# Kernel optimization log

Hardware: AMD Instinct MI355X
Metric: run time of the kernel (lower is better)

## Reference

```python
import jax, jax.numpy as jnp
import numpy as np

EPS = 1e-5
ND, NDIS, NP, NG, NPW = 40000, 40000, 80000, 80000, 40000
D = 128


def gcn(x_src, src, dst, n_dst, W, b):
    # DGL GraphConv with norm='both': D_dst^{-1/2} A^T D_src^{-1/2} X W + b
    deg_out = jnp.maximum(jnp.zeros((x_src.shape[0],), x_src.dtype).at[src].add(1.0), 1.0)
    xs = x_src * (deg_out ** -0.5)[:, None]
    msg = jax.ops.segment_sum(xs[src], dst, num_segments=n_dst)
    deg_in = jnp.maximum(jnp.zeros((n_dst,), x_src.dtype).at[dst].add(1.0), 1.0)
    return (msg * (deg_in ** -0.5)[:, None]) @ W + b


def bn_prelu(v, gamma, beta, a):
    # BatchNorm1d (training-mode batch stats, biased var) then PReLU (scalar slope)
    mu = v.mean(0)
    var = v.var(0)
    y = gamma * (v - mu) / jnp.sqrt(var + EPS) + beta
    return jnp.where(y >= 0, y, a * y)


def sem_att(z, W1, b1, w2):
    # z: [N, K, D]; shared SemanticAttention across node types
    s = jnp.tanh(z @ W1 + b1) @ w2        # [N, K]
    beta = jax.nn.softmax(s.mean(0))       # [K]
    return jnp.einsum('k,nkd->nd', beta, z)


def setup_inputs():
    key = jax.random.key(0)
    ks = iter(jax.random.split(key, 40))
    f = lambda n: jax.random.normal(next(ks), (n, D), jnp.float32)
    inp = {'h_drug': f(ND), 'h_disease': f(NDIS), 'h_protein': f(NP),
           'h_gene': f(NG), 'h_pathway': f(NPW)}
    rels = {'dd': (ND, ND, 640000), 'ddi': (ND, NDIS, 640000), 'disdis': (NDIS, NDIS, 640000),
            'dp': (ND, NP, 640000), 'pp': (NP, NP, 1280000), 'pg': (NP, NG, 1280000),
            'gg': (NG, NG, 1280000), 'gpw': (NG, NPW, 1280000), 'pwpw': (NPW, NPW, 640000),
            'pwdis': (NPW, NDIS, 640000)}
    for name, (ns, nd, E) in rels.items():
        inp[name + '_src'] = jax.random.randint(next(ks), (E,), 0, ns)
        inp[name + '_dst'] = jax.random.randint(next(ks), (E,), 0, nd)
    inp['W_blocks'] = jax.random.normal(next(ks), (5, 3, D, D), jnp.float32) * 0.09
    inp['b_blocks'] = jnp.zeros((5, 3, D), jnp.float32)
    inp['bn_gamma'] = jnp.ones((5, D), jnp.float32)
    inp['bn_beta'] = jnp.zeros((5, D), jnp.float32)
    inp['prelu_a'] = jnp.full((5,), 0.25, jnp.float32)
    inp['attn_W1'] = jax.random.normal(next(ks), (D, D), jnp.float32) * 0.09
    inp['attn_b1'] = jnp.zeros((D,), jnp.float32)
    inp['attn_w2'] = jax.random.normal(next(ks), (D,), jnp.float32) * 0.09
    return inp


def reference(h_drug, h_disease, h_protein, h_gene, h_pathway,
              dd_src, dd_dst, ddi_src, ddi_dst, disdis_src, disdis_dst,
              dp_src, dp_dst, pp_src, pp_dst, pg_src, pg_dst,
              gg_src, gg_dst, gpw_src, gpw_dst, pwpw_src, pwpw_dst,
              pwdis_src, pwdis_dst,
              W_blocks, b_blocks, bn_gamma, bn_beta, prelu_a,
              attn_W1, attn_b1, attn_w2):
    act = lambda i, v: bn_prelu(v, bn_gamma[i], bn_beta[i], prelu_a[i])
    # block 0: drug_disease  (rels: drug_drug, drug_disease, disease_disease)
    d0 = act(0, gcn(h_drug, dd_src, dd_dst, ND, W_blocks[0, 0], b_blocks[0, 0]))
    dis0 = act(0, gcn(h_drug, ddi_src, ddi_dst, NDIS, W_blocks[0, 1], b_blocks[0, 1])
               + gcn(h_disease, disdis_src, disdis_dst, NDIS, W_blocks[0, 2], b_blocks[0, 2]))
    # block 1: drug_protein
    d1 = act(1, gcn(h_drug, dd_src, dd_dst, ND, W_blocks[1, 0], b_blocks[1, 0]))
    p1 = act(1, gcn(h_drug, dp_src, dp_dst, NP, W_blocks[1, 1], b_blocks[1, 1])
             + gcn(h_protein, pp_src, pp_dst, NP, W_blocks[1, 2], b_blocks[1, 2]))
    # block 2: protein_gene
    p2 = act(2, gcn(h_protein, pp_src, pp_dst, NP, W_blocks[2, 0], b_blocks[2, 0]))
    g2 = act(2, gcn(h_protein, pg_src, pg_dst, NG, W_blocks[2, 1], b_blocks[2, 1])
             + gcn(h_gene, gg_src, gg_dst, NG, W_blocks[2, 2], b_blocks[2, 2]))
    # block 3: gene_pathway
    g3 = act(3, gcn(h_gene, gg_src, gg_dst, NG, W_blocks[3, 0], b_blocks[3, 0]))
    pw3 = act(3, gcn(h_gene, gpw_src, gpw_dst, NPW, W_blocks[3, 1], b_blocks[3, 1])
              + gcn(h_pathway, pwpw_src, pwpw_dst, NPW, W_blocks[3, 2], b_blocks[3, 2]))
    # block 4: pathway_disease
    pw4 = act(4, gcn(h_pathway, pwpw_src, pwpw_dst, NPW, W_blocks[4, 0], b_blocks[4, 0]))
    dis4 = act(4, gcn(h_pathway, pwdis_src, pwdis_dst, NDIS, W_blocks[4, 1], b_blocks[4, 1])
               + gcn(h_disease, disdis_src, disdis_dst, NDIS, W_blocks[4, 2], b_blocks[4, 2]))
    att = lambda a, b: sem_att(jnp.stack([a, b], axis=1), attn_W1, attn_b1, attn_w2)
    return (att(d0, d1), att(dis0, dis4), att(p1, p2), att(g2, g3), att(pw3, pw4))
```

## Files before the change

kernel.cpp:

```cpp
#include <hip/hip_runtime.h>
#include <hip/hip_bf16.h>

#define D128 128

typedef __attribute__((ext_vector_type(8))) short bf16x8;
typedef __attribute__((ext_vector_type(4))) float f32x4;

__device__ inline unsigned short f2bf(float f) {
    unsigned u = __float_as_uint(f);
    u = u + 0x7fffu + ((u >> 16) & 1u);
    return (unsigned short)(u >> 16);
}
__device__ inline float bf2f(unsigned short h) {
    return __uint_as_float(((unsigned)h) << 16);
}
__device__ inline float fast_tanh(float x) {
    float e = __expf(2.f * x);
    return 1.f - 2.f * __builtin_amdgcn_rcpf(e + 1.f);
}

__device__ __forceinline__ void stage_w(const unsigned short* __restrict__ Wt,
                                        unsigned short* lw, int t)
{
    const uint4* srcW = (const uint4*)Wt;
    uint4* dstW = (uint4*)lw;
    for (int i = t; i < 2048; i += 256) {
        int row = i >> 4, sl = i & 15;
        dstW[row * 16 + (sl ^ (row & 7))] = srcW[i];
    }
}
__device__ __forceinline__ bf16x8 read_w(const unsigned short* lw, int row, int kt, int lq)
{
    int slot = (kt * 4 + lq) ^ (row & 7);
    return *(const bf16x8*)(lw + row * 128 + slot * 8);
}

__device__ __forceinline__ void wave_scan(const int* arr, int* ofs, int n, int lane)
{
    int k = (n + 63) >> 6;
    int base = lane * k;
    int sum = 0;
    for (int i = 0; i < k; i++) { int idx = base + i; if (idx < n) sum += arr[idx]; }
    int pre = sum;
    for (int off = 1; off < 64; off <<= 1) {
        int u = __shfl(pre, (lane - off) & 63);
        if (lane >= off) pre += u;
    }
    int run = pre - sum;
    for (int i = 0; i < k; i++) { int idx = base + i; if (idx < n) { ofs[idx] = run; run += arr[idx]; } }
    if (lane == 63) ofs[n] = run;
}

__global__ __launch_bounds__(256) void xconv_scaled(
    const float* __restrict__ in, const int* __restrict__ degs,
    unsigned* __restrict__ out, int nrows)
{
    int t = threadIdx.x;
    int lane = t & 63, rr = t >> 6;
    int row = blockIdx.x * 4 + rr;
    if (row >= nrows) return;
    float sc = rsqrtf((float)max(degs[row], 1));
    float2 v = ((const float2*)(in + (size_t)row * 128))[lane];
    out[(size_t)row * 64 + lane] =
        (unsigned)f2bf(v.x * sc) | ((unsigned)f2bf(v.y * sc) << 16);
}

__global__ void wconv_t(const float* __restrict__ W_blocks, const float* __restrict__ W1,
                        unsigned short* __restrict__ wt)
{
    int m = blockIdx.x;
    const float* src = (m < 15) ? (W_blocks + (size_t)m * 16384) : W1;
    unsigned short* dst = wt + (size_t)m * 16384;
    for (int i = threadIdx.x; i < 16384; i += 256) {
        int n = i >> 7, k = i & 127;
        dst[i] = f2bf(src[k * 128 + n]);
    }
}

struct BuildArgs {
    const int* esrc[10]; const int* edst[10];
    int* histD; int* histS;
    int cumBlk[11]; int dstColBase[11]; int srcColBase[11]; int E[10];
};

__global__ __launch_bounds__(256) void part_count(BuildArgs A)
{
    __shared__ int hd[160], hs[320];
    int blk = blockIdx.x, t = threadIdx.x;
    int r = 0;
    while (r < 9 && blk >= A.cumBlk[r + 1]) r++;
    int blkInRel = blk - A.cumBlk[r];
    int nbD = A.dstColBase[r + 1] - A.dstColBase[r];
    int nbS = A.srcColBase[r + 1] - A.srcColBase[r];
    for (int i = t; i < nbD; i += 256) hd[i] = 0;
    for (int i = t; i < nbS; i += 256) hs[i] = 0;
    __syncthreads();
    int e0 = blkInRel * 16384;
    const int* sp = A.esrc[r];
    const int* dp = A.edst[r];
    int E = A.E[r];
#pragma unroll 4
    for (int j = 0; j < 64; j++) {
        int e = e0 + j * 256 + t;
        if (e < E) {
            atomicAdd(&hd[dp[e] >> 9], 1);
            atomicAdd(&hs[sp[e] >> 8], 1);
        }
    }
    __syncthreads();
    int cd = A.dstColBase[r], cs = A.srcColBase[r];
    for (int i = t; i < nbD; i += 256)
        A.histD[(size_t)(cd + i) * 80 + blkInRel] = hd[i];
    for (int i = t; i < nbS; i += 256)
        A.histS[(size_t)(cs + i) * 80 + blkInRel] = hs[i];
}

struct ScanArgs { int* hist; int* totals; int colBase[11]; int cumBlk[11]; };

__global__ __launch_bounds__(256) void col_scan(ScanArgs A)
{
    __shared__ int v[80];
    int col = blockIdx.x, t = threadIdx.x;
    int r = 0;
    while (r < 9 && col >= A.colBase[r + 1]) r++;
    int nblk = A.cumBlk[r + 1] - A.cumBlk[r];
    for (int i = t; i < nblk; i += 256) v[i] = A.hist[(size_t)col * 80 + i];
    __syncthreads();
    if (t == 0) {
        int run = 0;
        for (int i = 0; i < nblk; i++) { int c = v[i]; v[i] = run; run += c; }
        A.totals[col] = run;
    }
    __syncthreads();
    for (int i = t; i < nblk; i += 256) A.hist[(size_t)col * 80 + i] = v[i];
}

__global__ __launch_bounds__(256) void base_scan(const int* __restrict__ totals,
                                                 int* __restrict__ colbase, int n)
{
    __shared__ int v[2200];
    int t = threadIdx.x;
    for (int i = t; i < n; i += 256) v[i] = totals[i];
    __syncthreads();
    if (t == 0) {
        int run = 0;
        for (int i = 0; i < n; i++) { int c = v[i]; v[i] = run; run += c; }
        v[n] = run;
    }
    __syncthreads();
    for (int i = t; i <= n; i += 256) colbase[i] = v[i];
}

struct ScatArgs {
    const int* esrc[10]; const int* edst[10];
    const int* histD; const int* colbaseD;
    const int* histS; const int* colbaseS;
    int* epart; unsigned char* spart;
    int cumBlk[11]; int dstColBase[11]; int srcColBase[11]; int E[10];
};

__global__ __launch_bounds__(256) void scatter_all(ScatArgs A)
{
    __shared__ int stageE[4096];
    __shared__ unsigned short bidS[4096];
    __shared__ unsigned char bidE[4096];
    __shared__ unsigned char stageS[4096];
    __shared__ int gbaseD[160], gcurD[160], lhistD[160], lofsD[161];
    __shared__ int gbaseS[320], gcurS[320], lhistS[320], lofsS[321];

    int blk = blockIdx.x, t = threadIdx.x;
    int r = 0;
    while (r < 9 && blk >= A.cumBlk[r + 1]) r++;
    int blkInRel = blk - A.cumBlk[r];
    int cd = A.dstColBase[r], cs = A.srcColBase[r];
    int nbD = A.dstColBase[r + 1] - cd;
    int nbS = A.srcColBase[r + 1] - cs;
    for (int i = t; i < nbD; i += 256) {
        gbaseD[i] = A.colbaseD[cd + i] + A.histD[(size_t)(cd + i) * 80 + blkInRel];
        gcurD[i] = 0;
    }
    for (int i = t; i < nbS; i += 256) {
        gbaseS[i] = A.colbaseS[cs + i] + A.histS[(size_t)(cs + i) * 80 + blkInRel];
        gcurS[i] = 0;
    }
    const int* sp = A.esrc[r];
    const int* dp = A.edst[r];
    int E = A.E[r];
    int blkbase = blkInRel * 16384;

    for (int c = 0; c < 4; c++) {
        int e0 = blkbase + c * 4096;
        int sv[16], dv[16];
#pragma unroll
        for (int j = 0; j < 16; j++) {
            int e = e0 + j * 256 + t;
            sv[j] = (e < E) ? sp[e] : -1;
            dv[j] = (e < E) ? dp[e] : 0;
        }
        for (int i = t; i < nbD; i += 256) lhistD[i] = 0;
        for (int i = t; i < nbS; i += 256) lhistS[i] = 0;
        __syncthreads();
#pragma unroll
        for (int j = 0; j < 16; j++) {
            if (sv[j] >= 0) {
                atomicAdd(&lhistD[dv[j] >> 9], 1);
                atomicAdd(&lhistS[sv[j] >> 8], 1);
            }
        }
        __syncthreads();
        if (t < 64) wave_scan(lhistD, lofsD, nbD, t);
        else if (t < 128) wave_scan(lhistS, lofsS, nbS, t - 64);
        __syncthreads();
        for (int i = t; i < nbD; i += 256) lhistD[i] = 0;
        for (int i = t; i < nbS; i += 256) lhistS[i] = 0;
        __syncthreads();
#pragma unroll
        for (int j = 0; j < 16; j++) {
            if (sv[j] >= 0) {
                int bd = dv[j] >> 9;
                int p = atomicAdd(&lhistD[bd], 1);
                int ix = lofsD[bd] + p;
                stageE[ix] = (sv[j] & 0x1FFFF) | ((dv[j] & 511) << 17);
                bidE[ix] = (unsigned char)bd;
                int bs = sv[j] >> 8;
                int q = atomicAdd(&lhistS[bs], 1);
                int iy = lofsS[bs] + q;
                stageS[iy] = (unsigned char)(sv[j] & 255);
                bidS[iy] = (unsigned short)bs;
            }
        }
        __syncthreads();
        int cntv = lofsD[nbD];
        for (int i = t; i < cntv; i += 256) {
            int b = bidE[i];
            A.epart[gbaseD[b] + gcurD[b] + i - lofsD[b]] = stageE[i];
        }
        for (int i = t; i < cntv; i += 256) {
            int b = bidS[i];
            A.spart[(size_t)gbaseS[b] + gcurS[b] + i - lofsS[b]] = stageS[i];
        }
        __syncthreads();
        for (int i = t; i < nbD; i += 256) gcurD[i] += lofsD[i + 1] - lofsD[i];
        for (int i = t; i < nbS; i += 256) gcurS[i] += lofsS[i + 1] - lofsS[i];
        __syncthreads();
    }
}

struct FillArgs {
    const int* epart; const int* colbase;
    int* cursor; int* ebuf; int* oflow;
    int colBase[11];
    int cursorBase[10]; int ebufBase[10]; int cap[10]; int nd[10];
};

__global__ __launch_bounds__(256) void bucket_fill(FillArgs A)
{
    __shared__ int lcur[512];
    int col = blockIdx.x, t = threadIdx.x;
    int r = 0;
    while (r < 9 && col >= A.colBase[r + 1]) r++;
    int b = col - A.colBase[r];
    for (int i = t; i < 512; i += 256) lcur[i] = 0;
    __syncthreads();
    int start = A.colbase[col], end = A.colbase[col + 1];
    int cap = A.cap[r];
    int* eb = A.ebuf + (size_t)A.ebufBase[r];
    int* ofl = A.oflow + r * 8194;
    for (int i = start + t; i < end; i += 256) {
        int v = A.epart[i];
        int s = v & 0x1FFFF;
        int dlow = (v >> 17) & 511;
        int p = atomicAdd(&lcur[dlow], 1);
        if (p < cap) eb[(size_t)(b * 512 + dlow) * cap + p] = s;
        else {
            int q = atomicAdd(&ofl[0], 1);
            if (q < 4095) { ofl[2 + 2 * q] = b * 512 + dlow; ofl[3 + 2 * q] = s; }
        }
    }
    __syncthreads();
    for (int i = t; i < 512; i += 256) {
        int d = b * 512 + i;
        if (d < A.nd[r]) A.cursor[A.cursorBase[r] + d] = lcur[i];
    }
}

struct DegArgs {
    const unsigned char* spart; const int* colbase;
    int* degs;
    int colBase[11]; int degsBase[10]; int ns[10];
};

__global__ __launch_bounds__(256) void deg_count(DegArgs A)
{
    __shared__ int lc[256];
    int col = blockIdx.x, t = threadIdx.x;
    int r = 0;
    while (r < 9 && col >= A.colBase[r + 1]) r++;
    int b = col - A.colBase[r];
    lc[t] = 0;
    __syncthreads();
    int start = A.colbase[col], end = A.colbase[col + 1];
    for (int i = start + t; i < end; i += 256)
        atomicAdd(&lc[A.spart[i]], 1);
    __syncthreads();
    int s = b * 256 + t;
    if (s < A.ns[r]) A.degs[A.degsBase[r] + s] = lc[t];
}

__global__ __launch_bounds__(256) void gather_bf16(
    const unsigned* __restrict__ Xb,
    const int* __restrict__ cursor, const int* __restrict__ ebuf,
    const int* __restrict__ oflow, unsigned* __restrict__ aggb, int nd, int cap)
{
    int t = threadIdx.x;
    int lane = t & 63, r = t >> 6;
    int d = blockIdx.x * 4 + r;
    if (d >= nd) return;
    int cnt = cursor[d];
    int end = min(cnt, cap);
    const int* eb = ebuf + (size_t)d * cap;
    float a0 = 0.f, a1 = 0.f;
    int i = 0;
    for (; i + 4 <= end; i += 4) {
        int s0 = eb[i], s1 = eb[i + 1], s2 = eb[i + 2], s3 = eb[i + 3];
        unsigned x0 = Xb[(size_t)s0 * 64 + lane];
        unsigned x1 = Xb[(size_t)s1 * 64 + lane];
        unsigned x2 = Xb[(size_t)s2 * 64 + lane];
        unsigned x3 = Xb[(size_t)s3 * 64 + lane];
        a0 += bf2f((unsigned short)(x0 & 0xffff)) + bf2f((unsigned short)(x1 & 0xffff))
            + bf2f((unsigned short)(x2 & 0xffff)) + bf2f((unsigned short)(x3 & 0xffff));
        a1 += bf2f((unsigned short)(x0 >> 16)) + bf2f((unsigned short)(x1 >> 16))
            + bf2f((unsigned short)(x2 >> 16)) + bf2f((unsigned short)(x3 >> 16));
    }
    for (; i < end; i++) {
        int s0 = eb[i];
        unsigned x0 = Xb[(size_t)s0 * 64 + lane];
        a0 += bf2f((unsigned short)(x0 & 0xffff));
        a1 += bf2f((unsigned short)(x0 >> 16));
    }
    if (cnt > cap) {
        int n = min(oflow[0], 4095);
        for (int ii = 0; ii < n; ii++) {
            if (oflow[2 + 2 * ii] == d) {
                int s0 = oflow[3 + 2 * ii];
                unsigned x0 = Xb[(size_t)s0 * 64 + lane];
                a0 += bf2f((unsigned short)(x0 & 0xffff));
                a1 += bf2f((unsigned short)(x0 >> 16));
            }
        }
    }
    float sc = rsqrtf((float)max(cnt, 1));
    a0 *= sc; a1 *= sc;
    aggb[(size_t)d * 64 + lane] = (unsigned)f2bf(a0) | ((unsigned)f2bf(a1) << 16);
}

__device__ __forceinline__ void epi_store(
    f32x4* acc, unsigned short* __restrict__ Vb, int accum, int do_stats,
    float* ssum, float* ssq, int row0, int lr, int lq)
{
#pragma unroll
    for (int n = 0; n < 8; n++) {
        int col = n * 16 + lr;
        float s_ = 0.f, q_ = 0.f;
#pragma unroll
        for (int reg = 0; reg < 4; reg++) {
            int row = row0 + lq * 4 + reg;
            float v = acc[n][reg];
            unsigned short* vp = &Vb[(size_t)row * D128 + col];
            if (accum) v += bf2f(*vp);
            *vp = f2bf(v);
            s_ += v; q_ += v * v;
        }
        if (do_stats) {
            s_ += __shfl_xor(s_, 16); s_ += __shfl_xor(s_, 32);
            q_ += __shfl_xor(q_, 16); q_ += __shfl_xor(q_, 32);
            if (lq == 0) {
                atomicAdd(&ssum[col], s_);
                atomicAdd(&ssq[col], q_);
            }
        }
    }
}

__global__ __launch_bounds__(256) void gemm_mfma(
    const unsigned short* __restrict__ A, const unsigned short* __restrict__ Wt,
    unsigned short* __restrict__ Vb, int accum, int do_stats, float* __restrict__ statsraw)
{
    __shared__ unsigned short lw[16384];
    __shared__ float ssum[128], ssq[128];
    int t = threadIdx.x;
    int wave = t >> 6, lane = t & 63;
    int lr = lane & 15, lq = lane >> 4;
    int row0 = blockIdx.x * 64 + wave * 16;

    if (t < 128) { ssum[t] = 0.f; ssq[t] = 0.f; }
    stage_w(Wt, lw, t);
    __syncthreads();

    f32x4 acc[8];
#pragma unroll
    for (int n = 0; n < 8; n++) acc[n] = (f32x4)(0.f);

    const unsigned short* arow = A + (size_t)(row0 + lr) * 128 + lq * 8;
#pragma unroll
    for (int kt = 0; kt < 4; kt++) {
        bf16x8 af = *(const bf16x8*)(arow + kt * 32);
#pragma unroll
        for (int n = 0; n < 8; n++) {
            bf16x8 bfr = read_w(lw, n * 16 + lr, kt, lq);
            acc[n] = __builtin_amdgcn_mfma_f32_16x16x32_bf16(af, bfr, acc[n], 0, 0, 0);
        }
    }
    epi_store(acc, Vb, accum, do_stats, ssum, ssq, row0, lr, lq);
    if (do_stats) {
        __syncthreads();
        if (t < 128) atomicAdd(&statsraw[t], ssum[t]);
        else atomicAdd(&statsraw[t], ssq[t - 128]);
    }
}

__global__ __launch_bounds__(256) void gemm_mfma2(
    const unsigned short* __restrict__ A,
    const unsigned short* __restrict__ Wt0, const unsigned short* __restrict__ Wt1,
    unsigned short* __restrict__ V0b, unsigned short* __restrict__ V1b,
    int acc0f, int acc1f, int st0, int st1,
    float* __restrict__ sr0, float* __restrict__ sr1)
{
    __shared__ unsigned short lw0[16384], lw1[16384];
    __shared__ float ssum0[128], ssq0[128], ssum1[128], ssq1[128];
    int t = threadIdx.x;
    int wave = t >> 6, lane = t & 63;
    int lr = lane & 15, lq = lane >> 4;
    int row0 = blockIdx.x * 64 + wave * 16;

    if (t < 128) { ssum0[t] = 0.f; ssq0[t] = 0.f; ssum1[t] = 0.f; ssq1[t] = 0.f; }
    stage_w(Wt0, lw0, t);
    stage_w(Wt1, lw1, t);
    __syncthreads();

    f32x4 acc0[8], acc1[8];
#pragma unroll
    for (int n = 0; n < 8; n++) { acc0[n] = (f32x4)(0.f); acc1[n] = (f32x4)(0.f); }

    const unsigned short* arow = A + (size_t)(row0 + lr) * 128 + lq * 8;
#pragma unroll
    for (int kt = 0; kt < 4; kt++) {
        bf16x8 af = *(const bf16x8*)(arow + kt * 32);
#pragma unroll
        for (int n = 0; n < 8; n++) {
            int row = n * 16 + lr;
            bf16x8 b0 = read_w(lw0, row, kt, lq);
            bf16x8 b1 = read_w(lw1, row, kt, lq);
            acc0[n] = __builtin_amdgcn_mfma_f32_16x16x32_bf16(af, b0, acc0[n], 0, 0, 0);
            acc1[n] = __builtin_amdgcn_mfma_f32_16x16x32_bf16(af, b1, acc1[n], 0, 0, 0);
        }
    }
    epi_store(acc0, V0b, acc0f, st0, ssum0, ssq0, row0, lr, lq);
    epi_store(acc1, V1b, acc1f, st1, ssum1, ssq1, row0, lr, lq);
    __syncthreads();
    if (st0) {
        if (t < 128) atomicAdd(&sr0[t], ssum0[t]);
        else atomicAdd(&sr0[t], ssq0[t - 128]);
    }
    if (st1) {
        if (t < 128) atomicAdd(&sr1[t], ssum1[t]);
        else atomicAdd(&sr1[t], ssq1[t - 128]);
    }
}

struct FinArgs { int Ms[10]; };

__global__ void bn_finalize(const float* __restrict__ raw, float* __restrict__ fin, FinArgs fa)
{
    int tt = blockIdx.x;
    int c = threadIdx.x;
    float m = (float)fa.Ms[tt];
    float s = raw[tt * 256 + c], sq = raw[tt * 256 + 128 + c];
    float mu = s / m;
    float var = fmaxf(sq / m - mu * mu, 0.f);
    fin[tt * 256 + c] = mu;
    fin[tt * 256 + 128 + c] = rsqrtf(var + 1e-5f);
}

__global__ __launch_bounds__(256) void attn_t(
    const unsigned short* __restrict__ Vb, const float* __restrict__ raw, float Minv,
    const float* __restrict__ gam, const float* __restrict__ bet,
    const float* __restrict__ pa,
    const unsigned short* __restrict__ W1t, const float* __restrict__ b1,
    const float* __restrict__ w2, float* __restrict__ Sout)
{
    __shared__ float st[256];
    __shared__ float red[4];
    int t = threadIdx.x;
    if (t < 128) {
        float mu = raw[t] * Minv;
        float var = fmaxf(raw[128 + t] * Minv - mu * mu, 0.f);
        st[t] = mu;
        st[128 + t] = rsqrtf(var + 1e-5f);
    }
    __syncthreads();

    int wave = t >> 6, lane = t & 63;
    int lr = lane & 15, lq = lane >> 4;
    int row0 = blockIdx.x * 64 + wave * 16;
    float a = *pa;

    f32x4 acc[8];
#pragma unroll
    for (int n = 0; n < 8; n++) acc[n] = (f32x4)(0.f);

    const unsigned short* vrow = Vb + (size_t)(row0 + lr) * D128;
#pragma unroll
    for (int kt = 0; kt < 4; kt++) {
        int k0 = kt * 32 + lq * 8;
        bf16x8 vv = *(const bf16x8*)(vrow + k0);
        bf16x8 af;
#pragma unroll
        for (int jj = 0; jj < 8; jj++) {
            int cc = k0 + jj;
            float y = bf2f((unsigned short)vv[jj]);
            float yy = gam[cc] * (y - st[cc]) * st[128 + cc] + bet[cc];
            yy = yy >= 0.f ? yy : a * yy;
            af[jj] = (short)f2bf(yy);
        }
#pragma unroll
        for (int n = 0; n < 8; n++) {
            bf16x8 bfr = *(const bf16x8*)(W1t + (size_t)(n * 16 + lr) * 128 + k0);
            acc[n] = __builtin_amdgcn_mfma_f32_16x16x32_bf16(af, bfr, acc[n], 0, 0, 0);
        }
    }

    float thr = 0.f;
#pragma unroll
    for (int n = 0; n < 8; n++) {
        int col = n * 16 + lr;
        float bc = b1[col], wc = w2[col];
#pragma unroll
        for (int reg = 0; reg < 4; reg++)
            thr += fast_tanh(acc[n][reg] + bc) * wc;
    }
#pragma unroll
    for (int off = 1; off < 64; off <<= 1)
        thr += __shfl_xor(thr, off);
    if (lane == 0) red[wave] = thr;
    __syncthreads();
    if (t == 0) atomicAdd(Sout, red[0] + red[1] + red[2] + red[3]);
}

struct CombArgs {
    float* outp[5]; const unsigned short* va[5]; const unsigned short* vb[5];
    const float* stats; const float* gam; const float* bet; const float* pa; const float* S;
    int ta[5]; int tb[5]; int blka[5]; int blkb[5]; float invM[5]; int cum[6];
};

__global__ void combine_all(CombArgs D)
{
    int b = blockIdx.x, t = threadIdx.x;
    int p = 0;
    while (p < 4 && b >= D.cum[p + 1]) p++;
    size_t idx = (size_t)(b - D.cum[p]) * 256 + t;
    int c = (int)(idx & 127);
    float s0 = D.S[2 * p] * D.invM[p], s1 = D.S[2 * p + 1] * D.invM[p];
    float mx = fmaxf(s0, s1);
    float e0 = expf(s0 - mx), e1 = expf(s1 - mx);
    float inv = 1.f / (e0 + e1);
    float b0 = e0 * inv, b1w = e1 * inv;
    const float* sta = D.stats + D.ta[p] * 256;
    const float* stb = D.stats + D.tb[p] * 256;
    const float* ga = D.gam + D.blka[p] * 128;
    const float* ba = D.bet + D.blka[p] * 128;
    const float* gb = D.gam + D.blkb[p] * 128;
    const float* bb = D.bet + D.blkb[p] * 128;
    float aa = D.pa[D.blka[p]], ab = D.pa[D.blkb[p]];
    float va = bf2f(D.va[p][idx]);
    float vb = bf2f(D.vb[p][idx]);
    float ya = ga[c] * (va - sta[c]) * sta[128 + c] + ba[c];
    ya = ya >= 0.f ? ya : aa * ya;
    float yb = gb[c] * (vb - stb[c]) * stb[128 + c] + bb[c];
    yb = yb >= 0.f ? yb : ab * yb;
    D.outp[p][idx] = b0 * ya + b1w * yb;
}

extern "C" void kernel_launch(void* const* d_in, const int* in_sizes, int n_in,
                              void* d_out, int out_size, void* d_ws, size_t ws_size,
                              hipStream_t stream)
{
    const float* feats[5] = {
        (const float*)d_in[0], (const float*)d_in[1], (const float*)d_in[2],
        (const float*)d_in[3], (const float*)d_in[4]
    };
    const float* W_blocks = (const float*)d_in[25];
    const float* bn_gamma = (const float*)d_in[27];
    const float* bn_beta  = (const float*)d_in[28];
    const float* prelu_a  = (const float*)d_in[29];
    const float* attn_W1  = (const float*)d_in[30];
    const float* attn_b1  = (const float*)d_in[31];
    const float* attn_w2  = (const float*)d_in[32];
    float* out = (float*)d_out;

    unsigned* xbf  = (unsigned*)out;
    unsigned* aggb = (unsigned*)(out + 5120000);
    int*      ebuf = (int*)(out + 10240000);

    float* wsf = (float*)d_ws;
    unsigned short* wsvb = (unsigned short*)wsf;
    unsigned short* wtbf = (unsigned short*)(wsf + 35840000);
    int* degs     = (int*)(wsf + 35971072);
    int* cursor   = degs + 560000;
    int* oflow    = cursor + 560000;
    int* histD    = oflow + 81940;
    int* histS    = histD + 88160;
    int* colbaseD = histS + 175520;
    int* totalsD  = colbaseD + 1103;
    int* colbaseS = totalsD + 1102;
    int* totalsS  = colbaseS + 2195;
    int* epart    = totalsS + 2194;
    unsigned char* spart = (unsigned char*)(epart + 8960000);
    float* statsraw = (float*)(epart + 8960000 + 2240000);
    float* statsfin = statsraw + 2560;
    float* Ssum     = statsfin + 2560;
    size_t needed = ((size_t)((float*)(Ssum + 16) - wsf)) * 4;
    if (ws_size < needed) return;

    const int Mt[10]  = {40000, 40000, 40000, 40000, 80000, 80000, 80000, 80000, 40000, 40000};
    const int blk[10] = {0, 1, 0, 4, 1, 2, 2, 3, 3, 4};
    size_t offV[10];
    {
        size_t o = 0;
        for (int t = 0; t < 10; t++) { offV[t] = o; o += (size_t)Mt[t] * 128; }
    }
    unsigned short* Vb[10];
    for (int t = 0; t < 10; t++) Vb[t] = wsvb + offV[t];
    const size_t offT[5] = {0, 5120000, 10240000, 20480000, 30720000};

    const int relFeat[10] = {0, 0, 0, 1, 2, 2, 3, 3, 4, 4};
    const int relSrc[10]  = {5, 7, 11, 9, 13, 15, 17, 19, 21, 23};
    const int relNs[10]   = {40000, 40000, 40000, 40000, 80000, 80000, 80000, 80000, 40000, 40000};
    const int relNd[10]   = {40000, 40000, 80000, 40000, 80000, 80000, 80000, 40000, 40000, 40000};
    const int relE[10]    = {640000, 640000, 640000, 640000, 1280000,
                             1280000, 1280000, 1280000, 640000, 640000};
    const int relCap[10]  = {40, 40, 24, 40, 40, 40, 40, 56, 40, 40};
    const int cumBlk[11]  = {0, 40, 80, 120, 160, 239, 318, 397, 476, 516, 556};
    const int dstColBase[11] = {0, 79, 158, 315, 394, 551, 708, 865, 944, 1023, 1102};
    const int srcColBase[11] = {0, 157, 314, 471, 628, 941, 1254, 1567, 1880, 2037, 2194};
    const int degsBase[10]   = {0, 40000, 80000, 120000, 160000, 240000, 320000, 400000, 480000, 520000};
    const int cursorBase[10] = {0, 40000, 80000, 160000, 200000, 280000, 360000, 440000, 480000, 520000};
    const int ebufBase[10]   = {0, 1600000, 3200000, 5120000, 6720000, 9920000,
                                13120000, 16320000, 18560000, 20160000};

    struct GJob { int tid; int widx; int accum; int stats; };
    const int relNjob[10] = {2, 1, 1, 2, 2, 1, 2, 1, 2, 1};
    const GJob relJob[10][2] = {
        {{0,  0, 0, 1}, {1,  3, 0, 1}},
        {{2,  1, 0, 0}, {0,  0, 0, 0}},
        {{4,  4, 0, 0}, {0,  0, 0, 0}},
        {{2,  2, 1, 1}, {3, 14, 0, 0}},
        {{4,  5, 1, 1}, {5,  6, 0, 1}},
        {{6,  7, 0, 0}, {0,  0, 0, 0}},
        {{6,  8, 1, 1}, {7,  9, 0, 1}},
        {{8, 10, 0, 0}, {0,  0, 0, 0}},
        {{8, 11, 1, 1}, {9, 12, 0, 1}},
        {{3, 13, 1, 1}, {0,  0, 0, 0}},
    };
    const int doneCnt[10] = {2, 0, 0, 1, 2, 0, 2, 0, 2, 1};
    const int doneT[10][2] = {{0,1},{0,0},{0,0},{2,0},{4,5},{0,0},{6,7},{0,0},{8,9},{3,0}};

    wconv_t<<<16, 256, 0, stream>>>(W_blocks, attn_W1, wtbf);
    hipMemsetAsync(statsraw, 0, (2560 + 2560 + 16) * sizeof(float), stream);
    hipMemsetAsync(oflow, 0, (size_t)81940 * sizeof(int), stream);

    BuildArgs BA;
    ScanArgs  SAD, SAS;
    ScatArgs  CA;
    FillArgs  FA;
    DegArgs   DA;
    for (int r = 0; r < 10; r++) {
        BA.esrc[r] = (const int*)d_in[relSrc[r]];
        BA.edst[r] = (const int*)d_in[relSrc[r] + 1];
        BA.E[r] = relE[r];
        CA.esrc[r] = BA.esrc[r]; CA.edst[r] = BA.edst[r]; CA.E[r] = relE[r];
        FA.cursorBase[r] = cursorBase[r];
        FA.ebufBase[r] = ebufBase[r];
        FA.cap[r] = relCap[r];
        FA.nd[r] = relNd[r];
        DA.degsBase[r] = degsBase[r];
        DA.ns[r] = relNs[r];
    }
    for (int i = 0; i < 11; i++) {
        BA.cumBlk[i] = cumBlk[i]; BA.dstColBase[i] = dstColBase[i]; BA.srcColBase[i] = srcColBase[i];
        SAD.colBase[i] = dstColBase[i]; SAD.cumBlk[i] = cumBlk[i];
        SAS.colBase[i] = srcColBase[i]; SAS.cumBlk[i] = cumBlk[i];
        CA.cumBlk[i] = cumBlk[i]; CA.dstColBase[i] = dstColBase[i]; CA.srcColBase[i] = srcColBase[i];
        FA.colBase[i] = dstColBase[i];
        DA.colBase[i] = srcColBase[i];
    }
    BA.histD = histD; BA.histS = histS;
    SAD.hist = histD; SAD.totals = totalsD;
    SAS.hist = histS; SAS.totals = totalsS;
    CA.histD = histD; CA.colbaseD = colbaseD;
    CA.histS = histS; CA.colbaseS = colbaseS;
    CA.epart = epart; CA.spart = spart;
    FA.epart = epart; FA.colbase = colbaseD;
    FA.cursor = cursor; FA.ebuf = ebuf; FA.oflow = oflow;
    DA.spart = spart; DA.colbase = colbaseS; DA.degs = degs;

    part_count<<<556, 256, 0, stream>>>(BA);
    col_scan<<<1102, 256, 0, stream>>>(SAD);
    col_scan<<<2194, 256, 0, stream>>>(SAS);
    base_scan<<<1, 256, 0, stream>>>(totalsD, colbaseD, 1102);
    base_scan<<<1, 256, 0, stream>>>(totalsS, colbaseS, 2194);
    scatter_all<<<556, 256, 0, stream>>>(CA);
    bucket_fill<<<1102, 256, 0, stream>>>(FA);
    deg_count<<<2194, 256, 0, stream>>>(DA);

    for (int r = 0; r < 10; r++) {
        xconv_scaled<<<(relNs[r] + 3) / 4, 256, 0, stream>>>(
            feats[relFeat[r]], degs + degsBase[r], xbf, relNs[r]);
        gather_bf16<<<relNd[r] / 4, 256, 0, stream>>>(
            xbf, cursor + cursorBase[r],
            ebuf + (size_t)ebufBase[r], oflow + r * 8194, aggb, relNd[r], relCap[r]);
        if (relNjob[r] == 2) {
            const GJob& G0 = relJob[r][0];
            const GJob& G1 = relJob[r][1];
            gemm_mfma2<<<relNd[r] / 64, 256, 0, stream>>>(
                (const unsigned short*)aggb,
                wtbf + (size_t)G0.widx * 16384, wtbf + (size_t)G1.widx * 16384,
                Vb[G0.tid], Vb[G1.tid], G0.accum, G1.accum, G0.stats, G1.stats,
                statsraw + (size_t)G0.tid * 256, statsraw + (size_t)G1.tid * 256);
        } else {
            const GJob& G = relJob[r][0];
            gemm_mfma<<<relNd[r] / 64, 256, 0, stream>>>(
                (const unsigned short*)aggb, wtbf + (size_t)G.widx * 16384,
                Vb[G.tid], G.accum, G.stats, statsraw + (size_t)G.tid * 256);
        }
        for (int k = 0; k < doneCnt[r]; k++) {
            int t = doneT[r][k];
            attn_t<<<Mt[t] / 64, 256, 0, stream>>>(
                Vb[t], statsraw + (size_t)t * 256, 1.0f / Mt[t],
                bn_gamma + blk[t] * 128, bn_beta + blk[t] * 128, prelu_a + blk[t],
                wtbf + (size_t)15 * 16384, attn_b1, attn_w2, Ssum + t);
        }
    }

    FinArgs fa;
    for (int t = 0; t < 10; t++) fa.Ms[t] = Mt[t];
    bn_finalize<<<10, 128, 0, stream>>>(statsraw, statsfin, fa);

    CombArgs CD;
    CD.stats = statsfin; CD.gam = bn_gamma; CD.bet = bn_beta; CD.pa = prelu_a; CD.S = Ssum;
    CD.cum[0] = 0;
    for (int p = 0; p < 5; p++) {
        CD.outp[p] = out + offT[p];
        CD.va[p] = Vb[p * 2];
        CD.vb[p] = Vb[p * 2 + 1];
        CD.ta[p] = p * 2; CD.tb[p] = p * 2 + 1;
        CD.blka[p] = blk[p * 2]; CD.blkb[p] = blk[p * 2 + 1];
        CD.invM[p] = 1.0f / Mt[p * 2];
        CD.cum[p + 1] = CD.cum[p] + Mt[p * 2] / 2;
    }
    combine_all<<<CD.cum[5], 256, 0, stream>>>(CD);
}
```

Measured before the change: 1.548 ms.

## Fuse bucket fill into gather via per-block LDS counting sort of edges

```diff
diff --git a/kernel.cpp b/kernel.cpp
--- a/kernel.cpp
+++ b/kernel.cpp
@@ -2,6 +2,7 @@
 #include <hip/hip_bf16.h>
 
 #define D128 128
+#define STAGE 12288
 
 typedef __attribute__((ext_vector_type(8))) short bf16x8;
 typedef __attribute__((ext_vector_type(4))) float f32x4;
@@ -85,7 +86,7 @@
 
 __global__ __launch_bounds__(256) void part_count(BuildArgs A)
 {
-    __shared__ int hd[160], hs[320];
+    __shared__ int hd[320], hs[320];
     int blk = blockIdx.x, t = threadIdx.x;
     int r = 0;
     while (r < 9 && blk >= A.cumBlk[r + 1]) r++;
@@ -103,7 +104,7 @@
     for (int j = 0; j < 64; j++) {
         int e = e0 + j * 256 + t;
         if (e < E) {
-            atomicAdd(&hd[dp[e] >> 9], 1);
+            atomicAdd(&hd[dp[e] >> 8], 1);
             atomicAdd(&hs[sp[e] >> 8], 1);
         }
     }
@@ -162,10 +163,10 @@
 __global__ __launch_bounds__(256) void scatter_all(ScatArgs A)
 {
     __shared__ int stageE[4096];
+    __shared__ unsigned short bidE[4096];
     __shared__ unsigned short bidS[4096];
-    __shared__ unsigned char bidE[4096];
     __shared__ unsigned char stageS[4096];
-    __shared__ int gbaseD[160], gcurD[160], lhistD[160], lofsD[161];
+    __shared__ int gbaseD[320], gcurD[320], lhistD[320], lofsD[321];
     __shared__ int gbaseS[320], gcurS[320], lhistS[320], lofsS[321];
 
     int blk = blockIdx.x, t = threadIdx.x;
@@ -203,7 +204,7 @@
 #pragma unroll
         for (int j = 0; j < 16; j++) {
             if (sv[j] >= 0) {
-                atomicAdd(&lhistD[dv[j] >> 9], 1);
+                atomicAdd(&lhistD[dv[j] >> 8], 1);
                 atomicAdd(&lhistS[sv[j] >> 8], 1);
             }
         }
@@ -217,11 +218,11 @@
 #pragma unroll
         for (int j = 0; j < 16; j++) {
             if (sv[j] >= 0) {
-                int bd = dv[j] >> 9;
+                int bd = dv[j] >> 8;
                 int p = atomicAdd(&lhistD[bd], 1);
                 int ix = lofsD[bd] + p;
-                stageE[ix] = (sv[j] & 0x1FFFF) | ((dv[j] & 511) << 17);
-                bidE[ix] = (unsigned char)bd;
+                stageE[ix] = (sv[j] & 0x1FFFF) | ((dv[j] & 255) << 17);
+                bidE[ix] = (unsigned short)bd;
                 int bs = sv[j] >> 8;
                 int q = atomicAdd(&lhistS[bs], 1);
                 int iy = lofsS[bs] + q;
@@ -246,44 +247,6 @@
     }
 }
 
-struct FillArgs {
-    const int* epart; const int* colbase;
-    int* cursor; int* ebuf; int* oflow;
-    int colBase[11];
-    int cursorBase[10]; int ebufBase[10]; int cap[10]; int nd[10];
-};
-
-__global__ __launch_bounds__(256) void bucket_fill(FillArgs A)
-{
-    __shared__ int lcur[512];
-    int col = blockIdx.x, t = threadIdx.x;
-    int r = 0;
-    while (r < 9 && col >= A.colBase[r + 1]) r++;
-    int b = col - A.colBase[r];
-    for (int i = t; i < 512; i += 256) lcur[i] = 0;
-    __syncthreads();
-    int start = A.colbase[col], end = A.colbase[col + 1];
-    int cap = A.cap[r];
-    int* eb = A.ebuf + (size_t)A.ebufBase[r];
-    int* ofl = A.oflow + r * 8194;
-    for (int i = start + t; i < end; i += 256) {
-        int v = A.epart[i];
-        int s = v & 0x1FFFF;
-        int dlow = (v >> 17) & 511;
-        int p = atomicAdd(&lcur[dlow], 1);
-        if (p < cap) eb[(size_t)(b * 512 + dlow) * cap + p] = s;
-        else {
-            int q = atomicAdd(&ofl[0], 1);
-            if (q < 4095) { ofl[2 + 2 * q] = b * 512 + dlow; ofl[3 + 2 * q] = s; }
-        }
-    }
-    __syncthreads();
-    for (int i = t; i < 512; i += 256) {
-        int d = b * 512 + i;
-        if (d < A.nd[r]) A.cursor[A.cursorBase[r] + d] = lcur[i];
-    }
-}
-
 struct DegArgs {
     const unsigned char* spart; const int* colbase;
     int* degs;
@@ -307,51 +270,75 @@
     if (s < A.ns[r]) A.degs[A.degsBase[r] + s] = lc[t];
 }
 
-__global__ __launch_bounds__(256) void gather_bf16(
-    const unsigned* __restrict__ Xb,
-    const int* __restrict__ cursor, const int* __restrict__ ebuf,
-    const int* __restrict__ oflow, unsigned* __restrict__ aggb, int nd, int cap)
-{
-    int t = threadIdx.x;
-    int lane = t & 63, r = t >> 6;
-    int d = blockIdx.x * 4 + r;
-    if (d >= nd) return;
-    int cnt = cursor[d];
-    int end = min(cnt, cap);
-    const int* eb = ebuf + (size_t)d * cap;
-    float a0 = 0.f, a1 = 0.f;
-    int i = 0;
-    for (; i + 4 <= end; i += 4) {
-        int s0 = eb[i], s1 = eb[i + 1], s2 = eb[i + 2], s3 = eb[i + 3];
-        unsigned x0 = Xb[(size_t)s0 * 64 + lane];
-        unsigned x1 = Xb[(size_t)s1 * 64 + lane];
-        unsigned x2 = Xb[(size_t)s2 * 64 + lane];
-        unsigned x3 = Xb[(size_t)s3 * 64 + lane];
-        a0 += bf2f((unsigned short)(x0 & 0xffff)) + bf2f((unsigned short)(x1 & 0xffff))
-            + bf2f((unsigned short)(x2 & 0xffff)) + bf2f((unsigned short)(x3 & 0xffff));
-        a1 += bf2f((unsigned short)(x0 >> 16)) + bf2f((unsigned short)(x1 >> 16))
-            + bf2f((unsigned short)(x2 >> 16)) + bf2f((unsigned short)(x3 >> 16));
-    }
-    for (; i < end; i++) {
-        int s0 = eb[i];
-        unsigned x0 = Xb[(size_t)s0 * 64 + lane];
-        a0 += bf2f((unsigned short)(x0 & 0xffff));
-        a1 += bf2f((unsigned short)(x0 >> 16));
-    }
-    if (cnt > cap) {
-        int n = min(oflow[0], 4095);
-        for (int ii = 0; ii < n; ii++) {
-            if (oflow[2 + 2 * ii] == d) {
-                int s0 = oflow[3 + 2 * ii];
+__global__ __launch_bounds__(256) void bucket_gather(
+    const unsigned* __restrict__ Xb, const int* __restrict__ epart,
+    const int* __restrict__ colbase, int colBase0,
+    unsigned* __restrict__ aggb, int nd)
+{
+    __shared__ int stage[STAGE];
+    __shared__ int lhist[256], lofs[257];
+    int b = blockIdx.x, t = threadIdx.x;
+    int col = colBase0 + b;
+    int start = colbase[col], end = colbase[col + 1];
+    int total = end - start;
+    int main_ = min(total, STAGE);
+
+    lhist[t] = 0;
+    __syncthreads();
+    for (int i = t; i < main_; i += 256)
+        atomicAdd(&lhist[(epart[start + i] >> 17) & 255], 1);
+    __syncthreads();
+    if (t < 64) wave_scan(lhist, lofs, 256, t);
+    __syncthreads();
+    lhist[t] = 0;
+    __syncthreads();
+    for (int i = t; i < main_; i += 256) {
+        int v = epart[start + i];
+        int b8 = (v >> 17) & 255;
+        int p = atomicAdd(&lhist[b8], 1);
+        stage[lofs[b8] + p] = v & 0x1FFFF;
+    }
+    __syncthreads();
+
+    int lane = t & 63, sw = t >> 6;
+    for (int d8 = sw; d8 < 256; d8 += 4) {
+        int d = b * 256 + d8;
+        if (d >= nd) continue;
+        int sb = lofs[d8], se = lofs[d8 + 1];
+        int cnt = se - sb;
+        float a0 = 0.f, a1 = 0.f;
+        int i = sb;
+        for (; i + 4 <= se; i += 4) {
+            int s0 = stage[i], s1 = stage[i + 1], s2 = stage[i + 2], s3 = stage[i + 3];
+            unsigned x0 = Xb[(size_t)s0 * 64 + lane];
+            unsigned x1 = Xb[(size_t)s1 * 64 + lane];
+            unsigned x2 = Xb[(size_t)s2 * 64 + lane];
+            unsigned x3 = Xb[(size_t)s3 * 64 + lane];
+            a0 += bf2f((unsigned short)(x0 & 0xffff)) + bf2f((unsigned short)(x1 & 0xffff))
+                + bf2f((unsigned short)(x2 & 0xffff)) + bf2f((unsigned short)(x3 & 0xffff));
+            a1 += bf2f((unsigned short)(x0 >> 16)) + bf2f((unsigned short)(x1 >> 16))
+                + bf2f((unsigned short)(x2 >> 16)) + bf2f((unsigned short)(x3 >> 16));
+        }
+        for (; i < se; i++) {
+            int s0 = stage[i];
+            unsigned x0 = Xb[(size_t)s0 * 64 + lane];
+            a0 += bf2f((unsigned short)(x0 & 0xffff));
+            a1 += bf2f((unsigned short)(x0 >> 16));
+        }
+        for (int j = main_; j < total; j++) {
+            int v = epart[start + j];
+            if (((v >> 17) & 255) == d8) {
+                int s0 = v & 0x1FFFF;
                 unsigned x0 = Xb[(size_t)s0 * 64 + lane];
                 a0 += bf2f((unsigned short)(x0 & 0xffff));
                 a1 += bf2f((unsigned short)(x0 >> 16));
+                cnt++;
             }
         }
-    }
-    float sc = rsqrtf((float)max(cnt, 1));
-    a0 *= sc; a1 *= sc;
-    aggb[(size_t)d * 64 + lane] = (unsigned)f2bf(a0) | ((unsigned)f2bf(a1) << 16);
+        float sc = rsqrtf((float)max(cnt, 1));
+        a0 *= sc; a1 *= sc;
+        aggb[(size_t)d * 64 + lane] = (unsigned)f2bf(a0) | ((unsigned)f2bf(a1) << 16);
+    }
 }
 
 __device__ __forceinline__ void epi_store(
@@ -600,19 +587,16 @@
 
     unsigned* xbf  = (unsigned*)out;
     unsigned* aggb = (unsigned*)(out + 5120000);
-    int*      ebuf = (int*)(out + 10240000);
 
     float* wsf = (float*)d_ws;
     unsigned short* wsvb = (unsigned short*)wsf;
     unsigned short* wtbf = (unsigned short*)(wsf + 35840000);
     int* degs     = (int*)(wsf + 35971072);
-    int* cursor   = degs + 560000;
-    int* oflow    = cursor + 560000;
-    int* histD    = oflow + 81940;
-    int* histS    = histD + 88160;
+    int* histD    = degs + 560000;
+    int* histS    = histD + 175520;
     int* colbaseD = histS + 175520;
-    int* totalsD  = colbaseD + 1103;
-    int* colbaseS = totalsD + 1102;
+    int* totalsD  = colbaseD + 2195;
+    int* colbaseS = totalsD + 2194;
     int* totalsS  = colbaseS + 2195;
     int* epart    = totalsS + 2194;
     unsigned char* spart = (unsigned char*)(epart + 8960000);
@@ -639,14 +623,10 @@
     const int relNd[10]   = {40000, 40000, 80000, 40000, 80000, 80000, 80000, 40000, 40000, 40000};
     const int relE[10]    = {640000, 640000, 640000, 640000, 1280000,
                              1280000, 1280000, 1280000, 640000, 640000};
-    const int relCap[10]  = {40, 40, 24, 40, 40, 40, 40, 56, 40, 40};
     const int cumBlk[11]  = {0, 40, 80, 120, 160, 239, 318, 397, 476, 516, 556};
-    const int dstColBase[11] = {0, 79, 158, 315, 394, 551, 708, 865, 944, 1023, 1102};
+    const int dstColBase[11] = {0, 157, 314, 627, 784, 1097, 1410, 1723, 1880, 2037, 2194};
     const int srcColBase[11] = {0, 157, 314, 471, 628, 941, 1254, 1567, 1880, 2037, 2194};
     const int degsBase[10]   = {0, 40000, 80000, 120000, 160000, 240000, 320000, 400000, 480000, 520000};
-    const int cursorBase[10] = {0, 40000, 80000, 160000, 200000, 280000, 360000, 440000, 480000, 520000};
-    const int ebufBase[10]   = {0, 1600000, 3200000, 5120000, 6720000, 9920000,
-                                13120000, 16320000, 18560000, 20160000};
 
     struct GJob { int tid; int widx; int accum; int stats; };
     const int relNjob[10] = {2, 1, 1, 2, 2, 1, 2, 1, 2, 1};
@@ -667,22 +647,16 @@
 
     wconv_t<<<16, 256, 0, stream>>>(W_blocks, attn_W1, wtbf);
     hipMemsetAsync(statsraw, 0, (2560 + 2560 + 16) * sizeof(float), stream);
-    hipMemsetAsync(oflow, 0, (size_t)81940 * sizeof(int), stream);
 
     BuildArgs BA;
     ScanArgs  SAD, SAS;
     ScatArgs  CA;
-    FillArgs  FA;
     DegArgs   DA;
     for (int r = 0; r < 10; r++) {
         BA.esrc[r] = (const int*)d_in[relSrc[r]];
         BA.edst[r] = (const int*)d_in[relSrc[r] + 1];
         BA.E[r] = relE[r];
         CA.esrc[r] = BA.esrc[r]; CA.edst[r] = BA.edst[r]; CA.E[r] = relE[r];
-        FA.cursorBase[r] = cursorBase[r];
-        FA.ebufBase[r] = ebufBase[r];
-        FA.cap[r] = relCap[r];
-        FA.nd[r] = relNd[r];
         DA.degsBase[r] = degsBase[r];
         DA.ns[r] = relNs[r];
     }
@@ -691,7 +665,6 @@
         SAD.colBase[i] = dstColBase[i]; SAD.cumBlk[i] = cumBlk[i];
         SAS.colBase[i] = srcColBase[i]; SAS.cumBlk[i] = cumBlk[i];
         CA.cumBlk[i] = cumBlk[i]; CA.dstColBase[i] = dstColBase[i]; CA.srcColBase[i] = srcColBase[i];
-        FA.colBase[i] = dstColBase[i];
         DA.colBase[i] = srcColBase[i];
     }
     BA.histD = histD; BA.histS = histS;
@@ -700,25 +673,22 @@
     CA.histD = histD; CA.colbaseD = colbaseD;
     CA.histS = histS; CA.colbaseS = colbaseS;
     CA.epart = epart; CA.spart = spart;
-    FA.epart = epart; FA.colbase = colbaseD;
-    FA.cursor = cursor; FA.ebuf = ebuf; FA.oflow = oflow;
     DA.spart = spart; DA.colbase = colbaseS; DA.degs = degs;
 
     part_count<<<556, 256, 0, stream>>>(BA);
-    col_scan<<<1102, 256, 0, stream>>>(SAD);
+    col_scan<<<2194, 256, 0, stream>>>(SAD);
     col_scan<<<2194, 256, 0, stream>>>(SAS);
-    base_scan<<<1, 256, 0, stream>>>(totalsD, colbaseD, 1102);
+    base_scan<<<1, 256, 0, stream>>>(totalsD, colbaseD, 2194);
     base_scan<<<1, 256, 0, stream>>>(totalsS, colbaseS, 2194);
     scatter_all<<<556, 256, 0, stream>>>(CA);
-    bucket_fill<<<1102, 256, 0, stream>>>(FA);
     deg_count<<<2194, 256, 0, stream>>>(DA);
 
     for (int r = 0; r < 10; r++) {
         xconv_scaled<<<(relNs[r] + 3) / 4, 256, 0, stream>>>(
             feats[relFeat[r]], degs + degsBase[r], xbf, relNs[r]);
-        gather_bf16<<<relNd[r] / 4, 256, 0, stream>>>(
-            xbf, cursor + cursorBase[r],
-            ebuf + (size_t)ebufBase[r], oflow + r * 8194, aggb, relNd[r], relCap[r]);
+        int nbuck = dstColBase[r + 1] - dstColBase[r];
+        bucket_gather<<<nbuck, 256, 0, stream>>>(
+            xbf, epart, colbaseD, dstColBase[r], aggb, relNd[r]);
         if (relNjob[r] == 2) {
             const GJob& G0 = relJob[r][0];
             const GJob& G1 = relJob[r][1];
```

After: 2.520 ms. 62.8% more time.
